# Kernel optimization log

Measured on AMD Instinct MI355X. Metric: run time of the kernel, lower is better.

The kernel has to match this reference:

```python
import jax, jax.numpy as jnp
import numpy as np

MODEL_DIM = 1024
NUM_HEADS = 8
B, L = 16, 2048


def setup_inputs() -> dict:
    key = jax.random.key(0)
    ks = jax.random.split(key, 12)
    s = 1.0 / np.sqrt(MODEL_DIM)
    d = MODEL_DIM
    return {
        "query": jax.random.normal(ks[0], (B, L, d), jnp.float32),
        "key_": jax.random.normal(ks[1], (B, L, d), jnp.float32),
        "value": jax.random.normal(ks[2], (B, L, d), jnp.float32),
        "Wq": jax.random.uniform(ks[3], (d, d), jnp.float32, -s, s),
        "bq": jax.random.uniform(ks[4], (d,), jnp.float32, -s, s),
        "Wk": jax.random.uniform(ks[5], (d, d), jnp.float32, -s, s),
        "bk": jax.random.uniform(ks[6], (d,), jnp.float32, -s, s),
        "Wv": jax.random.uniform(ks[7], (d, d), jnp.float32, -s, s),
        "bv": jax.random.uniform(ks[8], (d,), jnp.float32, -s, s),
        "Wo": jax.random.uniform(ks[9], (d, d), jnp.float32, -s, s),
        "bo": jax.random.uniform(ks[10], (d,), jnp.float32, -s, s),
    }


def reference(query, key_, value, Wq, bq, Wk, bk, Wv, bv, Wo, bo):
    # NOTE: the original module does NOT split heads; attention is over the
    # full model_dim per batch row. num_heads only enters via the scale.
    residual = query
    q = jnp.einsum("bld,de->ble", query, Wq) + bq
    k = jnp.einsum("bld,de->ble", key_, Wk) + bk
    v = jnp.einsum("bld,de->ble", value, Wv) + bv
    scale = (MODEL_DIM // NUM_HEADS) ** (-0.5)
    attn = jnp.einsum("bqd,bkd->bqk", q, k) * scale  # [B, L, L]
    attn = jax.nn.softmax(attn, axis=-1)
    ctx = jnp.einsum("bqk,bkd->bqd", attn, v)
    out = jnp.einsum("bld,de->ble", ctx, Wo) + bo  # dropout=0.0 -> identity
    return residual + out
```

## Files before the change

kernel.cpp:

```cpp
#include <hip/hip_runtime.h>
#include <cstdint>

#define B_ 16
#define L_ 2048
#define D_ 1024
#define BLROWS (B_ * L_)
#define QK_SCALE 0.08838834764831845f

typedef unsigned short u16;
typedef __attribute__((ext_vector_type(8))) __bf16 bf16x8;
typedef __attribute__((ext_vector_type(4))) float f32x4;
typedef __attribute__((ext_vector_type(4))) unsigned int u32x4;
typedef __attribute__((ext_vector_type(4))) u16 u16x4;

__device__ __forceinline__ u16 f2bf(float f) {
  unsigned u = __builtin_bit_cast(unsigned, f);
  u += 0x7fffu + ((u >> 16) & 1u);
  return (u16)(u >> 16);
}
__device__ __forceinline__ float bf2f(unsigned hu) {
  return __builtin_bit_cast(float, hu << 16);
}

__device__ __forceinline__ void gll16(const void* g, void* l) {
  auto gp = reinterpret_cast<const __attribute__((address_space(1))) unsigned int*>(
      reinterpret_cast<uintptr_t>(g));
  auto lp = reinterpret_cast<__attribute__((address_space(3))) unsigned int*>(
      reinterpret_cast<uintptr_t>(l));
  __builtin_amdgcn_global_load_lds(gp, lp, 16, 0, 0);
}

typedef __attribute__((ext_vector_type(4))) float fv4;
__global__ void convert_bf16(const fv4* __restrict__ in, u16x4* __restrict__ out, int n4) {
  int i = blockIdx.x * blockDim.x + threadIdx.x;
  const int stride = gridDim.x * blockDim.x;
  for (; i < n4; i += stride) {
    fv4 v = in[i];
    u16x4 o;
    o.x = f2bf(v.x); o.y = f2bf(v.y); o.z = f2bf(v.z); o.w = f2bf(v.w);
    out[i] = o;
  }
}

__global__ void transpose_convert_1k(const float* __restrict__ W, u16* __restrict__ WT) {
  __shared__ float tile[32][33];
  const int bx = blockIdx.x * 32;
  const int by = blockIdx.y * 32;
  const int tx = threadIdx.x & 31;
  const int ty = threadIdx.x >> 5;
#pragma unroll
  for (int j = 0; j < 4; ++j) {
    const int r = ty + j * 8;
    tile[r][tx] = W[(size_t)(by + r) * 1024 + bx + tx];
  }
  __syncthreads();
#pragma unroll
  for (int j = 0; j < 4; ++j) {
    const int r = ty + j * 8;
    WT[(size_t)(bx + r) * 1024 + by + tx] = f2bf(tile[tx][r]);
  }
}

__global__ void softmax_rows(u16* __restrict__ S) {
  const size_t row = blockIdx.x;
  u32x4* p = (u32x4*)(S + row * 2048);
  const int t = threadIdx.x;
  u32x4 v = p[t];
  unsigned vv[4] = {v.x, v.y, v.z, v.w};
  float x[8];
#pragma unroll
  for (int i = 0; i < 4; ++i) {
    x[2 * i]     = bf2f(vv[i] & 0xffffu);
    x[2 * i + 1] = bf2f(vv[i] >> 16);
  }
  float m = x[0];
#pragma unroll
  for (int i = 1; i < 8; ++i) m = fmaxf(m, x[i]);
#pragma unroll
  for (int off = 32; off > 0; off >>= 1) m = fmaxf(m, __shfl_xor(m, off));
  __shared__ float red[4];
  const int w = t >> 6, l = t & 63;
  if (l == 0) red[w] = m;
  __syncthreads();
  m = fmaxf(fmaxf(red[0], red[1]), fmaxf(red[2], red[3]));
  float e[8], s = 0.f;
#pragma unroll
  for (int i = 0; i < 8; ++i) { e[i] = __expf(x[i] - m); s += e[i]; }
#pragma unroll
  for (int off = 32; off > 0; off >>= 1) s += __shfl_xor(s, off);
  __syncthreads();
  if (l == 0) red[w] = s;
  __syncthreads();
  s = red[0] + red[1] + red[2] + red[3];
  const float inv = 1.0f / s;
  unsigned oo[4];
#pragma unroll
  for (int i = 0; i < 4; ++i) {
    oo[i] = (unsigned)f2bf(e[2 * i] * inv) | ((unsigned)f2bf(e[2 * i + 1] * inv) << 16);
  }
  u32x4 o; o.x = oo[0]; o.y = oo[1]; o.z = oo[2]; o.w = oo[3];
  p[t] = o;
}

template <int OUT_BF16, int BIAS_MODE, int RESID>
__global__ void gemm_nt(const u16* __restrict__ A, const u16* __restrict__ Bm,
                        void* __restrict__ Cv, const float* __restrict__ bias,
                        const float* __restrict__ resid, int M, int N, int K, float scale,
                        long long sA, long long sB, long long sC) {
  __shared__ alignas(16) u16 lsA[128 * 32];
  __shared__ alignas(16) u16 lsB[128 * 32];

  const int z = blockIdx.z;
  A  += (long long)z * sA;
  Bm += (long long)z * sB;

  const int n0 = blockIdx.x * 128;
  const int m0 = blockIdx.y * 128;

  const int t = threadIdx.x;
  const int w = t >> 6;
  const int l = t & 63;
  const int lr = l & 15;
  const int lk = l >> 4;
  const int wr = w >> 1;
  const int wc = w & 1;

  const int srow = t >> 2;
  const int scol = (t & 3) * 8;
  const u16* ga0 = A + (long long)(m0 + srow) * K + scol;
  const u16* ga1 = ga0 + (long long)64 * K;
  const u16* gb0 = Bm + (long long)(n0 + srow) * K + scol;
  const u16* gb1 = gb0 + (long long)64 * K;
  char* lwa = (char*)lsA + w * 1024;
  char* lwb = (char*)lsB + w * 1024;

  f32x4 acc[4][4];
#pragma unroll
  for (int i = 0; i < 4; ++i)
#pragma unroll
    for (int j = 0; j < 4; ++j) acc[i][j] = f32x4{0.f, 0.f, 0.f, 0.f};

  for (int k0 = 0; k0 < K; k0 += 32) {
    __syncthreads();
    gll16(ga0 + k0, lwa);
    gll16(ga1 + k0, lwa + 4096);
    gll16(gb0 + k0, lwb);
    gll16(gb1 + k0, lwb + 4096);
    __syncthreads();

    bf16x8 af[4], bfr[4];
#pragma unroll
    for (int mi = 0; mi < 4; ++mi)
      af[mi] = __builtin_bit_cast(
          bf16x8, *(const u32x4*)&lsA[(wr * 64 + mi * 16 + lr) * 32 + lk * 8]);
#pragma unroll
    for (int ni = 0; ni < 4; ++ni)
      bfr[ni] = __builtin_bit_cast(
          bf16x8, *(const u32x4*)&lsB[(wc * 64 + ni * 16 + lr) * 32 + lk * 8]);
#pragma unroll
    for (int mi = 0; mi < 4; ++mi)
#pragma unroll
      for (int ni = 0; ni < 4; ++ni)
        acc[mi][ni] =
            __builtin_amdgcn_mfma_f32_16x16x32_bf16(af[mi], bfr[ni], acc[mi][ni], 0, 0, 0);
  }

#pragma unroll
  for (int mi = 0; mi < 4; ++mi) {
#pragma unroll
    for (int i = 0; i < 4; ++i) {
      const int grow = m0 + wr * 64 + mi * 16 + lk * 4 + i;
#pragma unroll
      for (int ni = 0; ni < 4; ++ni) {
        const int gcol = n0 + wc * 64 + ni * 16 + lr;
        float v = acc[mi][ni][i] * scale;
        if (BIAS_MODE == 1) v += bias[gcol];
        if (BIAS_MODE == 2) v += bias[grow];
        if (RESID) v += resid[(long long)grow * N + gcol];
        const long long cidx = (long long)z * sC + (long long)grow * N + gcol;
        if (OUT_BF16) ((u16*)Cv)[cidx] = f2bf(v);
        else          ((float*)Cv)[cidx] = v;
      }
    }
  }
}

extern "C" void kernel_launch(void* const* d_in, const int* in_sizes, int n_in,
                              void* d_out, int out_size, void* d_ws, size_t ws_size,
                              hipStream_t stream) {
  const float* query = (const float*)d_in[0];
  const float* key_  = (const float*)d_in[1];
  const float* value = (const float*)d_in[2];
  const float* Wq = (const float*)d_in[3];
  const float* bq = (const float*)d_in[4];
  const float* Wk = (const float*)d_in[5];
  const float* bk = (const float*)d_in[6];
  const float* Wv = (const float*)d_in[7];
  const float* bv = (const float*)d_in[8];
  const float* Wo = (const float*)d_in[9];
  const float* bo = (const float*)d_in[10];
  float* out = (float*)d_out;

  char* ws = (char*)d_ws;
  u16* xq  = (u16*)(ws + 0);
  u16* xk  = (u16*)(ws + 67108864);
  u16* xv  = (u16*)(ws + 134217728);
  u16* wqt = (u16*)(ws + 201326592);
  u16* wkt = (u16*)(ws + 203423744);
  u16* wvt = (u16*)(ws + 205520896);
  u16* wot = (u16*)(ws + 207618048);
  u16* qb  = (u16*)(ws + 209715200);
  u16* kb  = (u16*)(ws + 276824064);
  u16* vt  = (u16*)(ws + 343932928);
  u16* sp  = (u16*)(ws + 0);
  u16* ctx = (u16*)(ws + 134217728);

  const dim3 blk(256);
  const int n4 = BLROWS * D_ / 4;

  convert_bf16<<<2048, blk, 0, stream>>>((const fv4*)query, (u16x4*)xq, n4);
  convert_bf16<<<2048, blk, 0, stream>>>((const fv4*)key_,  (u16x4*)xk, n4);
  convert_bf16<<<2048, blk, 0, stream>>>((const fv4*)value, (u16x4*)xv, n4);
  transpose_convert_1k<<<dim3(32, 32), blk, 0, stream>>>(Wq, wqt);
  transpose_convert_1k<<<dim3(32, 32), blk, 0, stream>>>(Wk, wkt);
  transpose_convert_1k<<<dim3(32, 32), blk, 0, stream>>>(Wv, wvt);
  transpose_convert_1k<<<dim3(32, 32), blk, 0, stream>>>(Wo, wot);

  gemm_nt<1, 1, 0><<<dim3(8, 256, 1), blk, 0, stream>>>(
      xq, wqt, qb, bq, nullptr, BLROWS, D_, D_, 1.0f, 0, 0, 0);
  gemm_nt<1, 1, 0><<<dim3(8, 256, 1), blk, 0, stream>>>(
      xk, wkt, kb, bk, nullptr, BLROWS, D_, D_, 1.0f, 0, 0, 0);
  gemm_nt<1, 2, 0><<<dim3(16, 8, B_), blk, 0, stream>>>(
      wvt, xv, vt, bv, nullptr, D_, L_, D_, 1.0f,
      0, (long long)L_ * D_, (long long)D_ * L_);
  gemm_nt<1, 0, 0><<<dim3(16, 16, B_), blk, 0, stream>>>(
      qb, kb, sp, nullptr, nullptr, L_, L_, D_, QK_SCALE,
      (long long)L_ * D_, (long long)L_ * D_, (long long)L_ * L_);
  softmax_rows<<<BLROWS, blk, 0, stream>>>(sp);
  gemm_nt<1, 0, 0><<<dim3(8, 16, B_), blk, 0, stream>>>(
      sp, vt, ctx, nullptr, nullptr, L_, D_, L_, 1.0f,
      (long long)L_ * L_, (long long)D_ * L_, (long long)L_ * D_);
  gemm_nt<0, 1, 1><<<dim3(8, 256, 1), blk, 0, stream>>>(
      ctx, wot, out, bo, query, BLROWS, D_, D_, 1.0f, 0, 0, 0);

  (void)in_sizes; (void)n_in; (void)out_size; (void)ws_size;
}
```

Before: 1.244 ms.

## Replace GEMM with 256x256 double-buffered 8-wave kernel and XCD-aware tile mapping

```diff
diff --git a/kernel.cpp b/kernel.cpp
--- a/kernel.cpp
+++ b/kernel.cpp
@@ -102,78 +102,162 @@
   p[t] = o;
 }
 
+
+#define MFMA16(QM, QN, BF)                                                    \
+  _Pragma("unroll") for (int mf = 0; mf < 4; ++mf)                            \
+  _Pragma("unroll") for (int nf = 0; nf < 2; ++nf)                            \
+  _Pragma("unroll") for (int kk = 0; kk < 2; ++kk)                            \
+      acc[(QM)*4 + mf][(QN)*2 + nf] = __builtin_amdgcn_mfma_f32_16x16x32_bf16( \
+          af[mf][kk], BF[nf][kk], acc[(QM)*4 + mf][(QN)*2 + nf], 0, 0, 0);
+
 template <int OUT_BF16, int BIAS_MODE, int RESID>
-__global__ void gemm_nt(const u16* __restrict__ A, const u16* __restrict__ Bm,
-                        void* __restrict__ Cv, const float* __restrict__ bias,
-                        const float* __restrict__ resid, int M, int N, int K, float scale,
-                        long long sA, long long sB, long long sC) {
-  __shared__ alignas(16) u16 lsA[128 * 32];
-  __shared__ alignas(16) u16 lsB[128 * 32];
-
-  const int z = blockIdx.z;
+__global__ __launch_bounds__(512) void gemm8(
+    const u16* __restrict__ A, const u16* __restrict__ Bm, void* __restrict__ Cv,
+    const float* __restrict__ bias, const float* __restrict__ resid,
+    int N, int K, float scale, long long sA, long long sB, long long sC,
+    int gm, int gn) {
+  __shared__ alignas(16) u16 lds[2][4][128 * 64];
+
+  const int nwg = gridDim.x;
+  const int wg = blockIdx.x;
+  const int q = nwg >> 3, rr = nwg & 7;
+  const int xcd = wg & 7, idx = wg >> 3;
+  const int wgid = (xcd < rr ? xcd * (q + 1) : rr * (q + 1) + (xcd - rr) * q) + idx;
+  const int z = wgid / (gm * gn);
+  const int rem = wgid - z * gm * gn;
+  const int my = rem / gn;
+  const int nx = rem - my * gn;
+  const int m0 = my * 256, n0 = nx * 256;
+
   A  += (long long)z * sA;
   Bm += (long long)z * sB;
-
-  const int n0 = blockIdx.x * 128;
-  const int m0 = blockIdx.y * 128;
 
   const int t = threadIdx.x;
   const int w = t >> 6;
   const int l = t & 63;
+  const int wm = w >> 2;
+  const int wn = w & 3;
   const int lr = l & 15;
   const int lk = l >> 4;
-  const int wr = w >> 1;
-  const int wc = w & 1;
-
-  const int srow = t >> 2;
-  const int scol = (t & 3) * 8;
-  const u16* ga0 = A + (long long)(m0 + srow) * K + scol;
-  const u16* ga1 = ga0 + (long long)64 * K;
-  const u16* gb0 = Bm + (long long)(n0 + srow) * K + scol;
-  const u16* gb1 = gb0 + (long long)64 * K;
-  char* lwa = (char*)lsA + w * 1024;
-  char* lwb = (char*)lsB + w * 1024;
-
-  f32x4 acc[4][4];
-#pragma unroll
-  for (int i = 0; i < 4; ++i)
+
+  const int r  = t >> 3;
+  const int sl = (t & 7) ^ (r & 7);
+  const u16* pa00 = A  + (long long)(m0 +   0 + r) * K + sl * 8;
+  const u16* pa01 = A  + (long long)(m0 +  64 + r) * K + sl * 8;
+  const u16* pa10 = A  + (long long)(m0 + 128 + r) * K + sl * 8;
+  const u16* pa11 = A  + (long long)(m0 + 192 + r) * K + sl * 8;
+  const u16* pb00 = Bm + (long long)(n0 +   0 + r) * K + sl * 8;
+  const u16* pb01 = Bm + (long long)(n0 +  64 + r) * K + sl * 8;
+  const u16* pb10 = Bm + (long long)(n0 + 128 + r) * K + sl * 8;
+  const u16* pb11 = Bm + (long long)(n0 + 192 + r) * K + sl * 8;
+  const int wo = w * 512;
+
+#define STAGE_TILE_A(LB, KT)                         \
+  gll16(pa00 + (KT)*64, (LB) + 0 * 8192 +        wo); \
+  gll16(pa01 + (KT)*64, (LB) + 0 * 8192 + 4096 + wo); \
+  gll16(pa10 + (KT)*64, (LB) + 1 * 8192 +        wo); \
+  gll16(pa11 + (KT)*64, (LB) + 1 * 8192 + 4096 + wo);
+#define STAGE_TILE_B(LB, KT)                         \
+  gll16(pb00 + (KT)*64, (LB) + 2 * 8192 +        wo); \
+  gll16(pb01 + (KT)*64, (LB) + 2 * 8192 + 4096 + wo); \
+  gll16(pb10 + (KT)*64, (LB) + 3 * 8192 +        wo); \
+  gll16(pb11 + (KT)*64, (LB) + 3 * 8192 + 4096 + wo);
+
+  f32x4 acc[8][4];
+#pragma unroll
+  for (int i = 0; i < 8; ++i)
 #pragma unroll
     for (int j = 0; j < 4; ++j) acc[i][j] = f32x4{0.f, 0.f, 0.f, 0.f};
 
-  for (int k0 = 0; k0 < K; k0 += 32) {
-    __syncthreads();
-    gll16(ga0 + k0, lwa);
-    gll16(ga1 + k0, lwa + 4096);
-    gll16(gb0 + k0, lwb);
-    gll16(gb1 + k0, lwb + 4096);
-    __syncthreads();
-
-    bf16x8 af[4], bfr[4];
-#pragma unroll
-    for (int mi = 0; mi < 4; ++mi)
-      af[mi] = __builtin_bit_cast(
-          bf16x8, *(const u32x4*)&lsA[(wr * 64 + mi * 16 + lr) * 32 + lk * 8]);
-#pragma unroll
-    for (int ni = 0; ni < 4; ++ni)
-      bfr[ni] = __builtin_bit_cast(
-          bf16x8, *(const u32x4*)&lsB[(wc * 64 + ni * 16 + lr) * 32 + lk * 8]);
-#pragma unroll
-    for (int mi = 0; mi < 4; ++mi)
-#pragma unroll
-      for (int ni = 0; ni < 4; ++ni)
-        acc[mi][ni] =
-            __builtin_amdgcn_mfma_f32_16x16x32_bf16(af[mi], bfr[ni], acc[mi][ni], 0, 0, 0);
-  }
-
-#pragma unroll
-  for (int mi = 0; mi < 4; ++mi) {
+  const int cs0 = ((0 + lk) ^ (lr & 7)) * 8;
+  const int cs1 = ((4 + lk) ^ (lr & 7)) * 8;
+  const u16* LA = &lds[0][wm][0];
+  const u16* LB_ = &lds[0][2 + (wn >> 1)][0];
+  const int brow = (wn & 1) * 64 + lr;
+
+  {
+    u16* Lb = &lds[0][0][0];
+    STAGE_TILE_A(Lb, 0)
+    STAGE_TILE_B(Lb, 0)
+  }
+  asm volatile("s_waitcnt vmcnt(0)" ::: "memory");
+  __builtin_amdgcn_s_barrier();
+  __builtin_amdgcn_sched_barrier(0);
+
+  const int NT = K >> 6;
+  for (int kt = 0; kt < NT; ++kt) {
+    const int br = kt & 1, bs = br ^ 1;
+    const bool pf = (kt + 1 < NT);
+    const u16* Ra = LA + br * 32768;
+    const u16* Rb = LB_ + br * 32768;
+    u16* Lb = &lds[bs][0][0];
+
+    bf16x8 af[4][2], bf0[2][2], bf1[2][2];
+
+    if (pf) { STAGE_TILE_A(Lb, kt + 1) }
+#pragma unroll
+    for (int mf = 0; mf < 4; ++mf) {
+      const int row = mf * 16 + lr;
+      af[mf][0] = __builtin_bit_cast(bf16x8, *(const u32x4*)&Ra[row * 64 + cs0]);
+      af[mf][1] = __builtin_bit_cast(bf16x8, *(const u32x4*)&Ra[row * 64 + cs1]);
+    }
+#pragma unroll
+    for (int nf = 0; nf < 2; ++nf) {
+      const int row = brow + nf * 16;
+      bf0[nf][0] = __builtin_bit_cast(bf16x8, *(const u32x4*)&Rb[row * 64 + cs0]);
+      bf0[nf][1] = __builtin_bit_cast(bf16x8, *(const u32x4*)&Rb[row * 64 + cs1]);
+    }
+    __builtin_amdgcn_s_barrier();
+    __builtin_amdgcn_s_setprio(1);
+    MFMA16(0, 0, bf0)
+    __builtin_amdgcn_s_setprio(0);
+    __builtin_amdgcn_s_barrier();
+
+    if (pf) { STAGE_TILE_B(Lb, kt + 1) }
+#pragma unroll
+    for (int nf = 0; nf < 2; ++nf) {
+      const int row = brow + 32 + nf * 16;
+      bf1[nf][0] = __builtin_bit_cast(bf16x8, *(const u32x4*)&Rb[row * 64 + cs0]);
+      bf1[nf][1] = __builtin_bit_cast(bf16x8, *(const u32x4*)&Rb[row * 64 + cs1]);
+    }
+    __builtin_amdgcn_s_barrier();
+    __builtin_amdgcn_s_setprio(1);
+    MFMA16(0, 1, bf1)
+    __builtin_amdgcn_s_setprio(0);
+    __builtin_amdgcn_s_barrier();
+
+#pragma unroll
+    for (int mf = 0; mf < 4; ++mf) {
+      const int row = 64 + mf * 16 + lr;
+      af[mf][0] = __builtin_bit_cast(bf16x8, *(const u32x4*)&Ra[row * 64 + cs0]);
+      af[mf][1] = __builtin_bit_cast(bf16x8, *(const u32x4*)&Ra[row * 64 + cs1]);
+    }
+    __builtin_amdgcn_s_barrier();
+    __builtin_amdgcn_s_setprio(1);
+    MFMA16(1, 1, bf1)
+    __builtin_amdgcn_s_setprio(0);
+    __builtin_amdgcn_s_barrier();
+
+    __builtin_amdgcn_s_setprio(1);
+    MFMA16(1, 0, bf0)
+    __builtin_amdgcn_s_setprio(0);
+
+    if (pf) { asm volatile("s_waitcnt vmcnt(0)" ::: "memory"); }
+    __builtin_amdgcn_s_barrier();
+    __builtin_amdgcn_sched_barrier(0);
+  }
+
+  const int crow0 = m0 + wm * 128;
+  const int ccol0 = n0 + wn * 64;
+#pragma unroll
+  for (int mi = 0; mi < 8; ++mi) {
 #pragma unroll
     for (int i = 0; i < 4; ++i) {
-      const int grow = m0 + wr * 64 + mi * 16 + lk * 4 + i;
-#pragma unroll
-      for (int ni = 0; ni < 4; ++ni) {
-        const int gcol = n0 + wc * 64 + ni * 16 + lr;
-        float v = acc[mi][ni][i] * scale;
+      const int grow = crow0 + (mi >> 2) * 64 + (mi & 3) * 16 + lk * 4 + i;
+#pragma unroll
+      for (int nj = 0; nj < 4; ++nj) {
+        const int gcol = ccol0 + (nj >> 1) * 32 + (nj & 1) * 16 + lr;
+        float v = acc[mi][nj][i] * scale;
         if (BIAS_MODE == 1) v += bias[gcol];
         if (BIAS_MODE == 2) v += bias[grow];
         if (RESID) v += resid[(long long)grow * N + gcol];
@@ -216,6 +300,7 @@
   u16* ctx = (u16*)(ws + 134217728);
 
   const dim3 blk(256);
+  const dim3 blk8(512);
   const int n4 = BLROWS * D_ / 4;
 
   convert_bf16<<<2048, blk, 0, stream>>>((const fv4*)query, (u16x4*)xq, n4);
@@ -226,22 +311,22 @@
   transpose_convert_1k<<<dim3(32, 32), blk, 0, stream>>>(Wv, wvt);
   transpose_convert_1k<<<dim3(32, 32), blk, 0, stream>>>(Wo, wot);
 
-  gemm_nt<1, 1, 0><<<dim3(8, 256, 1), blk, 0, stream>>>(
-      xq, wqt, qb, bq, nullptr, BLROWS, D_, D_, 1.0f, 0, 0, 0);
-  gemm_nt<1, 1, 0><<<dim3(8, 256, 1), blk, 0, stream>>>(
-      xk, wkt, kb, bk, nullptr, BLROWS, D_, D_, 1.0f, 0, 0, 0);
-  gemm_nt<1, 2, 0><<<dim3(16, 8, B_), blk, 0, stream>>>(
-      wvt, xv, vt, bv, nullptr, D_, L_, D_, 1.0f,
-      0, (long long)L_ * D_, (long long)D_ * L_);
-  gemm_nt<1, 0, 0><<<dim3(16, 16, B_), blk, 0, stream>>>(
-      qb, kb, sp, nullptr, nullptr, L_, L_, D_, QK_SCALE,
-      (long long)L_ * D_, (long long)L_ * D_, (long long)L_ * L_);
+  gemm8<1, 1, 0><<<dim3(512), blk8, 0, stream>>>(
+      xq, wqt, qb, bq, nullptr, D_, D_, 1.0f, 0, 0, 0, 128, 4);
+  gemm8<1, 1, 0><<<dim3(512), blk8, 0, stream>>>(
+      xk, wkt, kb, bk, nullptr, D_, D_, 1.0f, 0, 0, 0, 128, 4);
+  gemm8<1, 2, 0><<<dim3(512), blk8, 0, stream>>>(
+      wvt, xv, vt, bv, nullptr, L_, D_, 1.0f,
+      0, (long long)L_ * D_, (long long)D_ * L_, 4, 8);
+  gemm8<1, 0, 0><<<dim3(1024), blk8, 0, stream>>>(
+      qb, kb, sp, nullptr, nullptr, L_, D_, QK_SCALE,
+      (long long)L_ * D_, (long long)L_ * D_, (long long)L_ * L_, 8, 8);
   softmax_rows<<<BLROWS, blk, 0, stream>>>(sp);
-  gemm_nt<1, 0, 0><<<dim3(8, 16, B_), blk, 0, stream>>>(
-      sp, vt, ctx, nullptr, nullptr, L_, D_, L_, 1.0f,
-      (long long)L_ * L_, (long long)D_ * L_, (long long)L_ * D_);
-  gemm_nt<0, 1, 1><<<dim3(8, 256, 1), blk, 0, stream>>>(
-      ctx, wot, out, bo, query, BLROWS, D_, D_, 1.0f, 0, 0, 0);
+  gemm8<1, 0, 0><<<dim3(512), blk8, 0, stream>>>(
+      sp, vt, ctx, nullptr, nullptr, D_, L_, 1.0f,
+      (long long)L_ * L_, (long long)D_ * L_, (long long)L_ * D_, 8, 4);
+  gemm8<0, 1, 1><<<dim3(512), blk8, 0, stream>>>(
+      ctx, wot, out, bo, query, D_, D_, 1.0f, 0, 0, 0, 128, 4);
 
   (void)in_sizes; (void)n_in; (void)out_size; (void)ws_size;
 }
```

Measured after the change: 1.070 ms. -14.0%, faster.
